# Kernel optimization log

Measured on AMD Instinct MI355X. Metric: run time of the kernel, lower is better.

## Reference

```python
import jax, jax.numpy as jnp
import numpy as np
import math

WS = 4
NUM_HEAD = 8
EPS = 1e-5


def _ln(x, g, b):
    m = jnp.mean(x, axis=-1, keepdims=True)
    v = jnp.mean((x - m) ** 2, axis=-1, keepdims=True)
    return (x - m) / jnp.sqrt(v + EPS) * g + b


def _win_part(img):
    # (bs,H,W,d) -> (bs, nw, ws*ws, d), windows row-major, patches row-major (matches F.unfold)
    bs, H, W, d = img.shape
    x = img.reshape(bs, H // WS, WS, W // WS, WS, d).transpose(0, 1, 3, 2, 4, 5)
    return x.reshape(bs, (H // WS) * (W // WS), WS * WS, d)


def _win_merge(win, H, W):
    # inverse of _win_part (matches window2image)
    bs, nw, npw, d = win.shape
    x = win.reshape(bs, H // WS, W // WS, WS, WS, d).transpose(0, 1, 3, 2, 4, 5)
    return x.reshape(bs, H, W, d)


def _build_mask(H, W):
    # faithful port of build_mask_for_shifted_wmsa (note the -1e-09 constant)
    i = jnp.arange(H)
    j = jnp.arange(W)
    rt = (i + WS // 2) // WS
    ct = (j + WS // 2) // WS
    val = (rt[:, None] * (H // WS) + ct[None, :] + 1).astype(jnp.float32)
    rolled = jnp.roll(val, (-(WS // 2), -(WS // 2)), (0, 1))
    c = rolled.reshape(H // WS, WS, W // WS, WS).transpose(0, 2, 1, 3).reshape(-1, WS * WS)
    valid = (c[:, :, None] == c[:, None, :]).astype(jnp.float32)
    mask = (1.0 - valid) * (-1e-09)          # (nw, npw, npw)
    return jnp.tile(mask, (NUM_HEAD, 1, 1))  # (nh*nw, npw, npw) as in torch .tile(num_head,1,1)


def _mhsa(x, qkv_w, qkv_b, out_w, out_b, mask=None):
    b, s, d = x.shape
    nh, hd = NUM_HEAD, d // NUM_HEAD
    qkv = x @ qkv_w + qkv_b
    q, k, v = jnp.split(qkv, 3, axis=-1)
    hsplit = lambda t: t.reshape(b, s, nh, hd).transpose(0, 2, 1, 3)
    q, k, v = hsplit(q), hsplit(k), hsplit(v)
    sc = jnp.einsum('bhqd,bhkd->bhqk', q, k) / math.sqrt(hd)
    if mask is not None:
        # torch adds (nh*nw,n,n) mask to (bs*nw*nh,n,n) scores; valid only for bs=1
        sc = (sc.reshape(b * nh, s, s) + mask).reshape(b, nh, s, s)
    p = jax.nn.softmax(sc, axis=-1)
    o = jnp.einsum('bhqk,bhkd->bhqd', p, v).transpose(0, 2, 1, 3).reshape(b, s, d)
    return o @ out_w + out_b


def setup_inputs() -> dict:
    key = jax.random.key(0)
    ks = jax.random.split(key, 16)
    d = 512
    s = 0.02
    inp = {
        'x': jax.random.normal(ks[0], (1, 16384, d), jnp.float32),
        'ln1_g': jnp.ones((d,)), 'ln1_b': jnp.zeros((d,)),
        'ln2_g': jnp.ones((d,)), 'ln2_b': jnp.zeros((d,)),
        'ln3_g': jnp.ones((d,)), 'ln3_b': jnp.zeros((d,)),
        'ln4_g': jnp.ones((d,)), 'ln4_b': jnp.zeros((d,)),
        'qkv1_w': jax.random.normal(ks[1], (d, 3 * d)) * s, 'qkv1_b': jnp.zeros((3 * d,)),
        'attnout1_w': jax.random.normal(ks[2], (d, d)) * s, 'attnout1_b': jnp.zeros((d,)),
        'qkv2_w': jax.random.normal(ks[3], (d, 3 * d)) * s, 'qkv2_b': jnp.zeros((3 * d,)),
        'attnout2_w': jax.random.normal(ks[4], (d, d)) * s, 'attnout2_b': jnp.zeros((d,)),
        'mlp1a_w': jax.random.normal(ks[5], (d, 4 * d)) * s, 'mlp1a_b': jnp.zeros((4 * d,)),
        'mlp1b_w': jax.random.normal(ks[6], (4 * d, d)) * s, 'mlp1b_b': jnp.zeros((d,)),
        'mlp2a_w': jax.random.normal(ks[7], (d, 4 * d)) * s, 'mlp2a_b': jnp.zeros((4 * d,)),
        'mlp2b_w': jax.random.normal(ks[8], (4 * d, d)) * s, 'mlp2b_b': jnp.zeros((d,)),
    }
    return inp


def reference(x, ln1_g, ln1_b, ln2_g, ln2_b, ln3_g, ln3_b, ln4_g, ln4_b,
              qkv1_w, qkv1_b, attnout1_w, attnout1_b,
              qkv2_w, qkv2_b, attnout2_w, attnout2_b,
              mlp1a_w, mlp1a_b, mlp1b_w, mlp1b_b,
              mlp2a_w, mlp2a_b, mlp2b_w, mlp2b_b):
    bs, num_patch, d = x.shape
    H = int(math.isqrt(num_patch))
    nw = (H // WS) ** 2
    npw = WS * WS

    # W-MSA branch
    x1 = _ln(x, ln1_g, ln1_b)
    win = _win_part(x1.reshape(bs, H, H, d))
    a1 = _mhsa(win.reshape(bs * nw, npw, d), qkv1_w, qkv1_b, attnout1_w, attnout1_b)
    res1 = x + a1.reshape(bs, num_patch, d)  # NOTE: window-flattened order residual (faithful)
    h1 = _ln(res1, ln2_g, ln2_b)
    out1 = (h1 @ mlp1a_w + mlp1a_b) @ mlp1b_w + mlp1b_b + res1  # no activation (faithful)

    # SW-MSA branch
    in2 = _ln(out1, ln3_g, ln3_b).reshape(bs, nw, npw, d)
    img2 = _win_merge(in2, H, H)
    sh = -WS // 2  # -2
    shifted = _win_part(jnp.roll(img2, (sh, sh), (1, 2)))
    mask = _build_mask(H, H)
    a2 = _mhsa(shifted.reshape(bs * nw, npw, d), qkv2_w, qkv2_b, attnout2_w, attnout2_b, mask)
    back = _win_part(jnp.roll(_win_merge(a2.reshape(bs, nw, npw, d), H, H), (WS // 2, WS // 2), (1, 2)))
    res2 = out1 + back.reshape(bs, num_patch, d)
    h2 = _ln(res2, ln4_g, ln4_b)
    out2 = (h2 @ mlp2a_w + mlp2a_b) @ mlp2b_w + mlp2b_b + res2
    return out2.reshape(bs, nw, npw, d)
```

## Files before the change

kernel.cpp:

```cpp
#include <hip/hip_runtime.h>

typedef unsigned short u16;
typedef __attribute__((ext_vector_type(4))) float f32x4;
typedef __attribute__((ext_vector_type(8))) short short8;
typedef __attribute__((ext_vector_type(8))) __bf16 bf16x8;

__device__ __forceinline__ float bf2f(u16 h) {
  union { unsigned int u; float f; } c;
  c.u = ((unsigned int)h) << 16;
  return c.f;
}
__device__ __forceinline__ u16 f2bf(float f) {
  union { float f; unsigned int u; } c;
  c.f = f;
  unsigned int u = c.u;
  return (u16)((u + 0x7fffu + ((u >> 16) & 1u)) >> 16);
}

typedef __attribute__((address_space(1))) const unsigned int gu32_t;
typedef __attribute__((address_space(3))) unsigned int lu32_t;
__device__ __forceinline__ void gload_lds16(const void* g, void* l) {
  __builtin_amdgcn_global_load_lds((gu32_t*)g, (lu32_t*)l, 16, 0, 0);
}

__device__ __forceinline__ int perm_winpart(int t) {
  const int w = t >> 4, p = t & 15;
  const int r = ((w >> 5) << 2) + (p >> 2);
  const int c = ((w & 31) << 2) + (p & 3);
  return (r << 7) + c;
}
__device__ __forceinline__ int perm_shift(int t, int sh) {
  const int w = t >> 4, p = t & 15;
  const int r = (((w >> 5) << 2) + (p >> 2) + sh) & 127;
  const int c = (((w & 31) << 2) + (p & 3) + sh) & 127;
  return ((((r >> 2) << 5) + (c >> 2)) << 4) + (((r & 3) << 2) + (c & 3));
}

__global__ __launch_bounds__(256) void transpose_to_bf16(
    const float* __restrict__ src, u16* __restrict__ dst, int K, int N) {
  __shared__ __align__(16) float tile[32][33];
  const int tx = threadIdx.x, ty = threadIdx.y;
  const int bn = blockIdx.x * 32, bk = blockIdx.y * 32;
#pragma unroll
  for (int i = 0; i < 32; i += 8)
    tile[ty + i][tx] = src[(size_t)(bk + ty + i) * N + bn + tx];
  __syncthreads();
#pragma unroll
  for (int i = 0; i < 32; i += 8)
    dst[(size_t)(bn + ty + i) * K + bk + tx] = f2bf(tile[tx][ty + i]);
}

template <int MODE>
__global__ __launch_bounds__(64) void ln_gather_kernel(
    const float* __restrict__ src, const float* __restrict__ gam,
    const float* __restrict__ bet, u16* __restrict__ out) {
  const int t = blockIdx.x, lane = threadIdx.x;
  const int s = (MODE == 1) ? perm_winpart(t) : perm_shift(t, 2);
  const float* row = src + (size_t)s * 512 + lane * 8;
  f32x4 v0 = *(const f32x4*)(row);
  f32x4 v1 = *(const f32x4*)(row + 4);
  float sum = v0[0] + v0[1] + v0[2] + v0[3] + v1[0] + v1[1] + v1[2] + v1[3];
#pragma unroll
  for (int o = 32; o; o >>= 1) sum += __shfl_xor(sum, o);
  const float m = sum * (1.f / 512.f);
  float vs = 0.f;
#pragma unroll
  for (int i = 0; i < 4; ++i) {
    float d0 = v0[i] - m, d1 = v1[i] - m;
    vs += d0 * d0 + d1 * d1;
  }
#pragma unroll
  for (int o = 32; o; o >>= 1) vs += __shfl_xor(vs, o);
  const float inv = rsqrtf(vs * (1.f / 512.f) + 1e-5f);
  const int cb = lane * 8;
  u16* orow = out + (size_t)t * 512 + cb;
#pragma unroll
  for (int i = 0; i < 4; ++i) {
    orow[i] = f2bf((v0[i] - m) * inv * gam[cb + i] + bet[cb + i]);
    orow[i + 4] = f2bf((v1[i] - m) * inv * gam[cb + i + 4] + bet[cb + i + 4]);
  }
}

template <int GM>
__global__ __launch_bounds__(64) void resadd_ln_kernel(
    const float* __restrict__ base, const u16* __restrict__ addbf,
    const float* __restrict__ gam, const float* __restrict__ bet,
    float* __restrict__ resout, u16* __restrict__ lnout) {
  const int t = blockIdx.x, lane = threadIdx.x;
  const int s = (GM == 0) ? t : perm_shift(t, 126);
  const float* brow = base + (size_t)t * 512 + lane * 8;
  const u16* arow = addbf + (size_t)s * 512 + lane * 8;
  f32x4 b0 = *(const f32x4*)(brow);
  f32x4 b1 = *(const f32x4*)(brow + 4);
  short8 a8 = *(const short8*)(arow);
  float v[8];
#pragma unroll
  for (int i = 0; i < 4; ++i) {
    v[i] = b0[i] + bf2f((u16)a8[i]);
    v[i + 4] = b1[i] + bf2f((u16)a8[i + 4]);
  }
  float sum = 0.f;
#pragma unroll
  for (int i = 0; i < 8; ++i) sum += v[i];
#pragma unroll
  for (int o = 32; o; o >>= 1) sum += __shfl_xor(sum, o);
  const float m = sum * (1.f / 512.f);
  float vs = 0.f;
#pragma unroll
  for (int i = 0; i < 8; ++i) {
    float d = v[i] - m;
    vs += d * d;
  }
#pragma unroll
  for (int o = 32; o; o >>= 1) vs += __shfl_xor(vs, o);
  const float inv = rsqrtf(vs * (1.f / 512.f) + 1e-5f);
  const int cb = lane * 8;
  float* rrow = resout + (size_t)t * 512 + cb;
  f32x4 r0 = {v[0], v[1], v[2], v[3]};
  f32x4 r1 = {v[4], v[5], v[6], v[7]};
  *(f32x4*)(rrow) = r0;
  *(f32x4*)(rrow + 4) = r1;
  u16* orow = lnout + (size_t)t * 512 + cb;
#pragma unroll
  for (int i = 0; i < 8; ++i)
    orow[i] = f2bf((v[i] - m) * inv * gam[cb + i] + bet[cb + i]);
}

__global__ __launch_bounds__(64) void attn_kernel(const u16* __restrict__ QKV,
                                                  u16* __restrict__ ATT) {
  __shared__ __align__(16) u16 Qs[16 * 64];
  __shared__ __align__(16) u16 Ks[16 * 64];
  __shared__ __align__(16) u16 Vs[16 * 64];
  __shared__ __align__(16) float Ps[16 * 16];
  const int w = blockIdx.x >> 3, h = blockIdx.x & 7;
  const int lane = threadIdx.x;
  const int p = lane >> 2, q4 = lane & 3;
  const size_t gbase = (size_t)(w * 16 + p) * 1536 + h * 64 + q4 * 16;
  const int lbase = p * 64 + q4 * 16;
  *(short8*)(Qs + lbase) = *(const short8*)(QKV + gbase);
  *(short8*)(Qs + lbase + 8) = *(const short8*)(QKV + gbase + 8);
  *(short8*)(Ks + lbase) = *(const short8*)(QKV + gbase + 512);
  *(short8*)(Ks + lbase + 8) = *(const short8*)(QKV + gbase + 520);
  *(short8*)(Vs + lbase) = *(const short8*)(QKV + gbase + 1024);
  *(short8*)(Vs + lbase + 8) = *(const short8*)(QKV + gbase + 1032);
  __syncthreads();
  float sc[4] = {0.f, 0.f, 0.f, 0.f};
  for (int d = 0; d < 64; ++d) {
    const float qv = bf2f(Qs[p * 64 + d]);
#pragma unroll
    for (int j = 0; j < 4; ++j) sc[j] += qv * bf2f(Ks[(q4 * 4 + j) * 64 + d]);
  }
#pragma unroll
  for (int j = 0; j < 4; ++j) sc[j] *= 0.125f;
  float mx = fmaxf(fmaxf(sc[0], sc[1]), fmaxf(sc[2], sc[3]));
  mx = fmaxf(mx, __shfl_xor(mx, 1));
  mx = fmaxf(mx, __shfl_xor(mx, 2));
  float e[4], sm = 0.f;
#pragma unroll
  for (int j = 0; j < 4; ++j) {
    e[j] = expf(sc[j] - mx);
    sm += e[j];
  }
  sm += __shfl_xor(sm, 1);
  sm += __shfl_xor(sm, 2);
  const float isv = 1.f / sm;
#pragma unroll
  for (int j = 0; j < 4; ++j) Ps[p * 16 + q4 * 4 + j] = e[j] * isv;
  __syncthreads();
  float o[16];
#pragma unroll
  for (int i = 0; i < 16; ++i) o[i] = 0.f;
  for (int k = 0; k < 16; ++k) {
    const float pk = Ps[p * 16 + k];
#pragma unroll
    for (int dd = 0; dd < 16; ++dd) o[dd] += pk * bf2f(Vs[k * 64 + q4 * 16 + dd]);
  }
  u16* orow = ATT + (size_t)(w * 16 + p) * 512 + h * 64 + q4 * 16;
#pragma unroll
  for (int dd = 0; dd < 16; ++dd) orow[dd] = f2bf(o[dd]);
}

template <int EPI>
__global__ __launch_bounds__(256, 4) void gemm_bf16(
    const u16* __restrict__ A, const u16* __restrict__ BT,
    const float* __restrict__ bias, const float* __restrict__ res,
    void* __restrict__ outp, int M, int N, int K) {
  __shared__ __align__(16) u16 As[128 * 32];
  __shared__ __align__(16) u16 Bs[128 * 32];
  const int tid = threadIdx.x;
  const int wave = tid >> 6;
  const int lane = tid & 63;
  const int bm0 = blockIdx.x * 128;
  const int bn0 = blockIdx.y * 128;
  const int wm = (wave >> 1) * 64;
  const int wn = (wave & 1) * 64;

  const f32x4 zero = {0.f, 0.f, 0.f, 0.f};
  f32x4 acc[4][4];
#pragma unroll
  for (int i = 0; i < 4; ++i)
#pragma unroll
    for (int j = 0; j < 4; ++j) acc[i][j] = zero;

  const int fr = lane & 15;
  const int fk = (lane >> 4) * 8;

  for (int k0 = 0; k0 < K; k0 += 32) {
#pragma unroll
    for (int j = 0; j < 2; ++j) {
      const int ebase = j * 256 + wave * 64;
      const int e = ebase + lane;
      const int row = e >> 2;
      const int kk = (((e & 3) ^ ((e >> 3) & 3)) << 3);
      gload_lds16(A + (size_t)(bm0 + row) * K + k0 + kk, As + ebase * 8);
      gload_lds16(BT + (size_t)(bn0 + row) * K + k0 + kk, Bs + ebase * 8);
    }
    __syncthreads();
    bf16x8 af[4], bfv[4];
#pragma unroll
    for (int i = 0; i < 4; ++i) {
      const int ro = wm + i * 16 + fr;
      af[i] = *(const bf16x8*)(As + ro * 32 + (fk ^ ((((ro >> 1) & 3)) << 3)));
    }
#pragma unroll
    for (int i = 0; i < 4; ++i) {
      const int rn = wn + i * 16 + fr;
      bfv[i] = *(const bf16x8*)(Bs + rn * 32 + (fk ^ ((((rn >> 1) & 3)) << 3)));
    }
#pragma unroll
    for (int mi = 0; mi < 4; ++mi)
#pragma unroll
      for (int ni = 0; ni < 4; ++ni)
        acc[mi][ni] = __builtin_amdgcn_mfma_f32_16x16x32_bf16(
            af[mi], bfv[ni], acc[mi][ni], 0, 0, 0);
    __syncthreads();
  }

  const int cr = (lane >> 4) * 4;
  const int cc = lane & 15;
#pragma unroll
  for (int mi = 0; mi < 4; ++mi) {
#pragma unroll
    for (int ni = 0; ni < 4; ++ni) {
      const int cg = bn0 + wn + ni * 16 + cc;
      const float bv2 = bias[cg];
#pragma unroll
      for (int r = 0; r < 4; ++r) {
        const int rg = bm0 + wm + mi * 16 + cr + r;
        float v = acc[mi][ni][r] + bv2;
        if (EPI == 1) {
          if (res) v += res[(size_t)rg * N + cg];
          ((float*)outp)[(size_t)rg * N + cg] = v;
        } else {
          ((u16*)outp)[(size_t)rg * N + cg] = f2bf(v);
        }
      }
    }
  }
}

extern "C" void kernel_launch(void* const* d_in, const int* in_sizes, int n_in,
                              void* d_out, int out_size, void* d_ws,
                              size_t ws_size, hipStream_t stream) {
  (void)in_sizes;
  (void)n_in;
  (void)out_size;
  (void)ws_size;
  const float* x = (const float*)d_in[0];
  const float* ln1_g = (const float*)d_in[1];
  const float* ln1_b = (const float*)d_in[2];
  const float* ln2_g = (const float*)d_in[3];
  const float* ln2_b = (const float*)d_in[4];
  const float* ln3_g = (const float*)d_in[5];
  const float* ln3_b = (const float*)d_in[6];
  const float* ln4_g = (const float*)d_in[7];
  const float* ln4_b = (const float*)d_in[8];
  const float* qkv1_w = (const float*)d_in[9];
  const float* qkv1_b = (const float*)d_in[10];
  const float* ao1_w = (const float*)d_in[11];
  const float* ao1_b = (const float*)d_in[12];
  const float* qkv2_w = (const float*)d_in[13];
  const float* qkv2_b = (const float*)d_in[14];
  const float* ao2_w = (const float*)d_in[15];
  const float* ao2_b = (const float*)d_in[16];
  const float* m1a_w = (const float*)d_in[17];
  const float* m1a_b = (const float*)d_in[18];
  const float* m1b_w = (const float*)d_in[19];
  const float* m1b_b = (const float*)d_in[20];
  const float* m2a_w = (const float*)d_in[21];
  const float* m2a_b = (const float*)d_in[22];
  const float* m2b_w = (const float*)d_in[23];
  const float* m2b_b = (const float*)d_in[24];

  char* ws = (char*)d_ws;
  u16* wt = (u16*)ws;
  u16* w_qkv1 = wt;
  u16* w_ao1 = wt + 786432;
  u16* w_qkv2 = wt + 1048576;
  u16* w_ao2 = wt + 1835008;
  u16* w_m1a = wt + 2097152;
  u16* w_m1b = wt + 3145728;
  u16* w_m2a = wt + 4194304;
  u16* w_m2b = wt + 5242880;
  u16* A1 = (u16*)(ws + 12582912);
  u16* ATT = A1;
  u16* A0 = (u16*)(ws + 29360128);
  u16* BIG = (u16*)(ws + 46137344);
  float* R1 = (float*)(ws + 113246208);
  float* O1 = (float*)(ws + 146800640);

  const dim3 tb(32, 8);
  transpose_to_bf16<<<dim3(48, 16), tb, 0, stream>>>(qkv1_w, w_qkv1, 512, 1536);
  transpose_to_bf16<<<dim3(16, 16), tb, 0, stream>>>(ao1_w, w_ao1, 512, 512);
  transpose_to_bf16<<<dim3(48, 16), tb, 0, stream>>>(qkv2_w, w_qkv2, 512, 1536);
  transpose_to_bf16<<<dim3(16, 16), tb, 0, stream>>>(ao2_w, w_ao2, 512, 512);
  transpose_to_bf16<<<dim3(64, 16), tb, 0, stream>>>(m1a_w, w_m1a, 512, 2048);
  transpose_to_bf16<<<dim3(16, 64), tb, 0, stream>>>(m1b_w, w_m1b, 2048, 512);
  transpose_to_bf16<<<dim3(64, 16), tb, 0, stream>>>(m2a_w, w_m2a, 512, 2048);
  transpose_to_bf16<<<dim3(16, 64), tb, 0, stream>>>(m2b_w, w_m2b, 2048, 512);

  ln_gather_kernel<1><<<16384, 64, 0, stream>>>(x, ln1_g, ln1_b, A1);
  gemm_bf16<0><<<dim3(128, 12), 256, 0, stream>>>(A1, w_qkv1, qkv1_b, nullptr,
                                                  BIG, 16384, 1536, 512);
  attn_kernel<<<8192, 64, 0, stream>>>(BIG, ATT);
  gemm_bf16<0><<<dim3(128, 4), 256, 0, stream>>>(ATT, w_ao1, ao1_b, nullptr, A0,
                                                 16384, 512, 512);
  resadd_ln_kernel<0><<<16384, 64, 0, stream>>>(x, A0, ln2_g, ln2_b, R1, A1);
  gemm_bf16<0><<<dim3(128, 16), 256, 0, stream>>>(A1, w_m1a, m1a_b, nullptr,
                                                  BIG, 16384, 2048, 512);
  gemm_bf16<1><<<dim3(128, 4), 256, 0, stream>>>(BIG, w_m1b, m1b_b, R1, O1,
                                                 16384, 512, 2048);

  ln_gather_kernel<2><<<16384, 64, 0, stream>>>(O1, ln3_g, ln3_b, A1);
  gemm_bf16<0><<<dim3(128, 12), 256, 0, stream>>>(A1, w_qkv2, qkv2_b, nullptr,
                                                  BIG, 16384, 1536, 512);
  attn_kernel<<<8192, 64, 0, stream>>>(BIG, ATT);
  gemm_bf16<0><<<dim3(128, 4), 256, 0, stream>>>(ATT, w_ao2, ao2_b, nullptr, A0,
                                                 16384, 512, 512);
  resadd_ln_kernel<1><<<16384, 64, 0, stream>>>(O1, A0, ln4_g, ln4_b, R1, A1);
  gemm_bf16<0><<<dim3(128, 16), 256, 0, stream>>>(A1, w_m2a, m2a_b, nullptr,
                                                  BIG, 16384, 2048, 512);
  gemm_bf16<1><<<dim3(128, 4), 256, 0, stream>>>(BIG, w_m2b, m2b_b, R1,
                                                 (float*)d_out, 16384, 512, 2048);
}
```

Baseline: 553.1 us.

## Double-buffer LDS tiles in bf16 GEMM to overlap global loads with MFMA

```diff
diff --git a/kernel.cpp b/kernel.cpp
--- a/kernel.cpp
+++ b/kernel.cpp
@@ -185,8 +185,8 @@
     const u16* __restrict__ A, const u16* __restrict__ BT,
     const float* __restrict__ bias, const float* __restrict__ res,
     void* __restrict__ outp, int M, int N, int K) {
-  __shared__ __align__(16) u16 As[128 * 32];
-  __shared__ __align__(16) u16 Bs[128 * 32];
+  __shared__ __align__(16) u16 As[2][128 * 32];
+  __shared__ __align__(16) u16 Bs[2][128 * 32];
   const int tid = threadIdx.x;
   const int wave = tid >> 6;
   const int lane = tid & 63;
@@ -205,27 +205,45 @@
   const int fr = lane & 15;
   const int fk = (lane >> 4) * 8;
 
-  for (int k0 = 0; k0 < K; k0 += 32) {
-#pragma unroll
-    for (int j = 0; j < 2; ++j) {
-      const int ebase = j * 256 + wave * 64;
-      const int e = ebase + lane;
-      const int row = e >> 2;
-      const int kk = (((e & 3) ^ ((e >> 3) & 3)) << 3);
-      gload_lds16(A + (size_t)(bm0 + row) * K + k0 + kk, As + ebase * 8);
-      gload_lds16(BT + (size_t)(bn0 + row) * K + k0 + kk, Bs + ebase * 8);
-    }
-    __syncthreads();
+  const int e0 = wave * 64 + lane;
+  const int e1 = 256 + wave * 64 + lane;
+  const int r0 = e0 >> 2, r1 = e1 >> 2;
+  const int kk0 = (((e0 & 3) ^ ((e0 >> 3) & 3)) << 3);
+  const int kk1 = (((e1 & 3) ^ ((e1 >> 3) & 3)) << 3);
+  const size_t arow0 = (size_t)(bm0 + r0) * K;
+  const size_t arow1 = (size_t)(bm0 + r1) * K;
+  const size_t brow0 = (size_t)(bn0 + r0) * K;
+  const size_t brow1 = (size_t)(bn0 + r1) * K;
+  const int lds0 = (wave * 64) * 8;
+  const int lds1 = (256 + wave * 64) * 8;
+
+  const int NT = K >> 5;
+
+#define STAGE(buf, kt)                                               \
+  do {                                                               \
+    const int kb = (kt) << 5;                                        \
+    gload_lds16(A + arow0 + kb + kk0, &As[buf][lds0]);               \
+    gload_lds16(A + arow1 + kb + kk1, &As[buf][lds1]);               \
+    gload_lds16(BT + brow0 + kb + kk0, &Bs[buf][lds0]);              \
+    gload_lds16(BT + brow1 + kb + kk1, &Bs[buf][lds1]);              \
+  } while (0)
+
+  STAGE(0, 0);
+  __syncthreads();
+
+  for (int t = 0; t < NT; ++t) {
+    const int cur = t & 1;
+    if (t + 1 < NT) STAGE(cur ^ 1, t + 1);
     bf16x8 af[4], bfv[4];
 #pragma unroll
     for (int i = 0; i < 4; ++i) {
       const int ro = wm + i * 16 + fr;
-      af[i] = *(const bf16x8*)(As + ro * 32 + (fk ^ ((((ro >> 1) & 3)) << 3)));
+      af[i] = *(const bf16x8*)(&As[cur][ro * 32 + (fk ^ ((((ro >> 1) & 3)) << 3))]);
     }
 #pragma unroll
     for (int i = 0; i < 4; ++i) {
       const int rn = wn + i * 16 + fr;
-      bfv[i] = *(const bf16x8*)(Bs + rn * 32 + (fk ^ ((((rn >> 1) & 3)) << 3)));
+      bfv[i] = *(const bf16x8*)(&Bs[cur][rn * 32 + (fk ^ ((((rn >> 1) & 3)) << 3))]);
     }
 #pragma unroll
     for (int mi = 0; mi < 4; ++mi)
@@ -235,6 +253,7 @@
             af[mi], bfv[ni], acc[mi][ni], 0, 0, 0);
     __syncthreads();
   }
+#undef STAGE
 
   const int cr = (lane >> 4) * 4;
   const int cc = lane & 15;
```

Result: no change. 562.0 us (+1.6%).
